# Kernel tuning notes

Measured on AMD Instinct MI355X. Metric: run time of the kernel, lower is better.

The kernel has to match this reference:

```python
import jax, jax.numpy as jnp
import numpy as np

TEMP = 0.2
EPS = 1e-12  # F.normalize eps


def setup_inputs() -> dict:
    key = jax.random.key(0)
    k1, k2 = jax.random.split(key)
    l, B, K, D = 4, 64, 32, 128
    emb_i = jax.random.normal(k1, (l, B, K, D), dtype=jnp.float32)
    emb_j = jax.random.normal(k2, (l, B, K, D), dtype=jnp.float32)
    joint_valid = jnp.ones((B, K), dtype=jnp.float32)
    return {"emb_i": emb_i, "emb_j": emb_j, "joint_valid": joint_valid}


def _l2norm(x):
    n = jnp.sqrt(jnp.sum(x * x, axis=-1, keepdims=True))
    return x / jnp.maximum(n, EPS)


def reference(emb_i, emb_j, joint_valid):
    l, B, K, D = emb_i.shape
    N = B * K
    z_i = _l2norm(emb_i.reshape(l, N, D))
    z_j = _l2norm(emb_j.reshape(l, N, D))
    reps = jnp.concatenate([z_i, z_j], axis=1)              # (l, 2N, D), unit rows
    # cosine similarity of unit vectors == matmul
    sim = jnp.einsum('lnd,lmd->lnm', reps, reps)            # (l, 2N, 2N)
    idx = jnp.arange(N)
    pos = sim[:, idx, idx + N]                              # diag offset +N, (l, N)
    # note: original code uses the SAME +N offset diagonal for both ij and ji
    positives = jnp.concatenate([pos, pos], axis=1)         # (l, 2N)
    neg_mask = 1.0 - jnp.eye(2 * N, dtype=sim.dtype)        # (2N, 2N)
    denom = jnp.sum(neg_mask[None] * jnp.exp(sim / TEMP), axis=2)  # (l, 2N)
    loss_partial = -jnp.log(jnp.exp(positives / TEMP) / denom)    # (l, 2N)
    joints_mask = joint_valid.reshape(1, 1, B, K)
    all_num = jnp.sum(joint_valid)
    loss = jnp.sum(loss_partial.reshape(l, 2, B, K) * joints_mask) / (2.0 * all_num)
    return loss
```

## Files before the change

kernel.cpp:

```cpp
#include <hip/hip_runtime.h>
#include <hip/hip_bf16.h>

typedef __attribute__((ext_vector_type(8))) short short8;
typedef __attribute__((ext_vector_type(4))) float floatx4;

#define NROWS 4096
#define NHALF 2048
#define DDIM  128
#define SQRT_SCALE 2.6857914f
#define LN2 0.69314718056f

#define WS_ROWPART_OFF 64
#define WS_DIAG_OFF   131136
#define WS_POS_OFF    147520
#define WS_Z_BYTE_OFF 655616

__device__ inline unsigned short f2bf(float f) {
    unsigned u = __builtin_bit_cast(unsigned, f);
    u += 0x7fffu + ((u >> 16) & 1u);
    return (unsigned short)(u >> 16);
}

__global__ __launch_bounds__(256) void k_norm(const float* __restrict__ emb_i,
                                              const float* __restrict__ emb_j,
                                              const float* __restrict__ jv,
                                              float* __restrict__ wsf,
                                              unsigned short* __restrict__ z) {
    int bx = blockIdx.x, tid = threadIdx.x;
    if (bx == 2048) {
        __shared__ float sred[256];
        float s = 0.f;
        #pragma unroll
        for (int i = 0; i < 8; ++i) s += jv[tid + 256 * i];
        sred[tid] = s; __syncthreads();
        for (int off = 128; off > 0; off >>= 1) {
            if (tid < off) sred[tid] += sred[tid + off];
            __syncthreads();
        }
        if (tid == 0) wsf[1] = sred[0];
        return;
    }
    if (bx == 0 && tid == 0) wsf[0] = 0.f;

    int wave = tid >> 6, lane = tid & 63, half = lane >> 5, sl = lane & 31;
    int r = bx * 8 + wave * 2 + half;
    int l = r >> 12, n = r & 4095;
    const float* src = (n < NHALF) ? (emb_i + ((size_t)l * NHALF + n) * DDIM)
                                   : (emb_j + ((size_t)l * NHALF + (n - NHALF)) * DDIM);
    float4 v = *(const float4*)(src + sl * 4);
    float ss = v.x * v.x + v.y * v.y + v.z * v.z + v.w * v.w;
    #pragma unroll
    for (int off = 1; off < 32; off <<= 1) ss += __shfl_xor(ss, off);
    float inv = SQRT_SCALE / fmaxf(sqrtf(ss), 1e-12f);
    unsigned p0 = ((unsigned)f2bf(v.y * inv) << 16) | (unsigned)f2bf(v.x * inv);
    unsigned p1 = ((unsigned)f2bf(v.w * inv) << 16) | (unsigned)f2bf(v.z * inv);
    *(uint2*)(z + (size_t)r * DDIM + sl * 4) = (uint2){p0, p1};
}

__global__ __launch_bounds__(256) void k_sim(const unsigned short* __restrict__ z,
                                             float* __restrict__ rowpart,
                                             float* __restrict__ diag,
                                             float* __restrict__ pos) {
    int bx = blockIdx.x, tid = threadIdx.x;
    int l = bx & 3, rb = (bx >> 2) & 15, cg = bx >> 6;
    int wave = tid >> 6, lane = tid & 63, m = lane & 15, quad = lane >> 4;
    const unsigned short* zl = z + (size_t)l * NROWS * DDIM;
    int l4 = l * NROWS;
    int R0 = rb * 256 + wave * 64;
    int C0 = cg * 512;

    short8 a[4][4];
    #pragma unroll
    for (int rs = 0; rs < 4; ++rs) {
        const unsigned short* p = zl + (size_t)(R0 + rs * 16 + m) * DDIM + quad * 8;
        #pragma unroll
        for (int kk = 0; kk < 4; ++kk) a[rs][kk] = *(const short8*)(p + kk * 32);
    }
    floatx4 rsum[4];
    #pragma unroll
    for (int rs = 0; rs < 4; ++rs) rsum[rs] = (floatx4){0.f, 0.f, 0.f, 0.f};

    const unsigned short* bp = zl + (size_t)(C0 + m) * DDIM + quad * 8;
    short8 bc[4], bn[4];
    #pragma unroll
    for (int k = 0; k < 4; ++k) bc[k] = *(const short8*)(bp + k * 32);

    #pragma unroll 2
    for (int cs = 0; cs < 32; ++cs) {
        if (cs < 31) {
            const unsigned short* q = bp + (size_t)(cs + 1) * 16 * DDIM;
            #pragma unroll
            for (int k = 0; k < 4; ++k) bn[k] = *(const short8*)(q + k * 32);
        }
        int c0 = C0 + cs * 16;
        #pragma unroll
        for (int rs = 0; rs < 4; ++rs) {
            floatx4 acc = (floatx4){0.f, 0.f, 0.f, 0.f};
            acc = __builtin_amdgcn_mfma_f32_16x16x32_bf16(a[rs][0], bc[0], acc, 0, 0, 0);
            acc = __builtin_amdgcn_mfma_f32_16x16x32_bf16(a[rs][1], bc[1], acc, 0, 0, 0);
            acc = __builtin_amdgcn_mfma_f32_16x16x32_bf16(a[rs][2], bc[2], acc, 0, 0, 0);
            acc = __builtin_amdgcn_mfma_f32_16x16x32_bf16(a[rs][3], bc[3], acc, 0, 0, 0);
            int rbase = R0 + rs * 16;
            if (c0 == rbase || c0 == (rbase ^ 2048)) {
                int c = m - (quad << 2);
                if (c >= 0 && c < 4)
                    ((c0 == rbase) ? diag : pos)[l4 + rbase + m] = acc[c];
            }
            rsum[rs][0] += __builtin_amdgcn_exp2f(acc[0]);
            rsum[rs][1] += __builtin_amdgcn_exp2f(acc[1]);
            rsum[rs][2] += __builtin_amdgcn_exp2f(acc[2]);
            rsum[rs][3] += __builtin_amdgcn_exp2f(acc[3]);
        }
        if (cs < 31) {
            #pragma unroll
            for (int k = 0; k < 4; ++k) bc[k] = bn[k];
        }
    }
    #pragma unroll
    for (int off = 1; off < 16; off <<= 1)
        #pragma unroll
        for (int rs = 0; rs < 4; ++rs)
            #pragma unroll
            for (int c = 0; c < 4; ++c)
                rsum[rs][c] += __shfl_xor(rsum[rs][c], off);
    if (m == 0) {
        #pragma unroll
        for (int rs = 0; rs < 4; ++rs)
            #pragma unroll
            for (int c = 0; c < 4; ++c) {
                int rg = R0 + rs * 16 + quad * 4 + c;
                rowpart[cg * 16384 + l4 + rg] = rsum[rs][c];
            }
    }
}

__global__ __launch_bounds__(256) void k_loss(const float* __restrict__ jv,
                                              const float* __restrict__ rowpart,
                                              const float* __restrict__ diag,
                                              const float* __restrict__ pos,
                                              float* __restrict__ wsf) {
    __shared__ float sred[256];
    int tid = threadIdx.x;
    int r = blockIdx.x * 256 + tid;
    int n = r & 4095;
    float tot = 0.f;
    #pragma unroll
    for (int g = 0; g < 8; ++g) tot += rowpart[g * 16384 + r];
    float denom = tot - __builtin_amdgcn_exp2f(diag[r]);
    float contrib = LN2 * (__builtin_amdgcn_logf(denom) - pos[r]);
    float local = contrib * jv[n & (NHALF - 1)];
    sred[tid] = local; __syncthreads();
    for (int off = 128; off > 0; off >>= 1) {
        if (tid < off) sred[tid] += sred[tid + off];
        __syncthreads();
    }
    if (tid == 0) atomicAdd(&wsf[0], sred[0]);
}

__global__ void k_final(const float* __restrict__ wsf, float* __restrict__ out) {
    if (threadIdx.x == 0) out[0] = wsf[0] / (2.f * wsf[1]);
}

extern "C" void kernel_launch(void* const* d_in, const int* in_sizes, int n_in,
                              void* d_out, int out_size, void* d_ws, size_t ws_size,
                              hipStream_t stream) {
    const float* emb_i = (const float*)d_in[0];
    const float* emb_j = (const float*)d_in[1];
    const float* jv    = (const float*)d_in[2];
    float* wsf     = (float*)d_ws;
    float* rowpart = wsf + WS_ROWPART_OFF;
    float* diag    = wsf + WS_DIAG_OFF;
    float* pos     = wsf + WS_POS_OFF;
    unsigned short* z = (unsigned short*)((char*)d_ws + WS_Z_BYTE_OFF);
    float* out = (float*)d_out;

    k_norm <<<2049, 256, 0, stream>>>(emb_i, emb_j, jv, wsf, z);
    k_sim  <<<512,  256, 0, stream>>>(z, rowpart, diag, pos);
    k_loss <<<64,   256, 0, stream>>>(jv, rowpart, diag, pos, wsf);
    k_final<<<1,    64,  0, stream>>>(wsf, out);
}
```

Before: 102.6 us.

## Fuse similarity, loss and final kernels using atomic grid counters

Merges the similarity, per-row loss reduction and final division into one kernel. The first 64 blocks spin on an agent-scope atomic counter until all 512 blocks have written their row partials, then compute the loss, and the last finishing block writes the output. This removes two kernel launches and their gaps. The B-tile loop is also restructured into explicit double buffering with two register sets. The spin-wait relies on all 512 blocks being co-resident or the waiting blocks being scheduled after the others, which risks deadlock or stalls if they are not.

```diff
diff --git a/kernel.cpp b/kernel.cpp
--- a/kernel.cpp
+++ b/kernel.cpp
@@ -40,7 +40,9 @@
         if (tid == 0) wsf[1] = sred[0];
         return;
     }
-    if (bx == 0 && tid == 0) wsf[0] = 0.f;
+    if (bx == 0 && tid == 0) {
+        wsf[0] = 0.f; wsf[2] = 0.f; wsf[3] = 0.f;
+    }
 
     int wave = tid >> 6, lane = tid & 63, half = lane >> 5, sl = lane & 31;
     int r = bx * 8 + wave * 2 + half;
@@ -57,10 +59,16 @@
     *(uint2*)(z + (size_t)r * DDIM + sl * 4) = (uint2){p0, p1};
 }
 
-__global__ __launch_bounds__(256) void k_sim(const unsigned short* __restrict__ z,
-                                             float* __restrict__ rowpart,
-                                             float* __restrict__ diag,
-                                             float* __restrict__ pos) {
+__global__ __launch_bounds__(256) void k_simloss(const unsigned short* __restrict__ z,
+                                                 float* __restrict__ wsf,
+                                                 const float* __restrict__ jv,
+                                                 float* __restrict__ out) {
+    float* rowpart = wsf + WS_ROWPART_OFF;
+    float* diag    = wsf + WS_DIAG_OFF;
+    float* pos     = wsf + WS_POS_OFF;
+    unsigned* cnt  = (unsigned*)&wsf[2];
+    unsigned* cnt2 = (unsigned*)&wsf[3];
+
     int bx = blockIdx.x, tid = threadIdx.x;
     int l = bx & 3, rb = (bx >> 2) & 15, cg = bx >> 6;
     int wave = tid >> 6, lane = tid & 63, m = lane & 15, quad = lane >> 4;
@@ -80,26 +88,15 @@
     #pragma unroll
     for (int rs = 0; rs < 4; ++rs) rsum[rs] = (floatx4){0.f, 0.f, 0.f, 0.f};
 
-    const unsigned short* bp = zl + (size_t)(C0 + m) * DDIM + quad * 8;
-    short8 bc[4], bn[4];
-    #pragma unroll
-    for (int k = 0; k < 4; ++k) bc[k] = *(const short8*)(bp + k * 32);
-
-    #pragma unroll 2
-    for (int cs = 0; cs < 32; ++cs) {
-        if (cs < 31) {
-            const unsigned short* q = bp + (size_t)(cs + 1) * 16 * DDIM;
-            #pragma unroll
-            for (int k = 0; k < 4; ++k) bn[k] = *(const short8*)(q + k * 32);
-        }
-        int c0 = C0 + cs * 16;
+    auto simstep = [&](short8* B, int cs_) {
+        int c0 = C0 + cs_ * 16;
         #pragma unroll
         for (int rs = 0; rs < 4; ++rs) {
             floatx4 acc = (floatx4){0.f, 0.f, 0.f, 0.f};
-            acc = __builtin_amdgcn_mfma_f32_16x16x32_bf16(a[rs][0], bc[0], acc, 0, 0, 0);
-            acc = __builtin_amdgcn_mfma_f32_16x16x32_bf16(a[rs][1], bc[1], acc, 0, 0, 0);
-            acc = __builtin_amdgcn_mfma_f32_16x16x32_bf16(a[rs][2], bc[2], acc, 0, 0, 0);
-            acc = __builtin_amdgcn_mfma_f32_16x16x32_bf16(a[rs][3], bc[3], acc, 0, 0, 0);
+            acc = __builtin_amdgcn_mfma_f32_16x16x32_bf16(a[rs][0], B[0], acc, 0, 0, 0);
+            acc = __builtin_amdgcn_mfma_f32_16x16x32_bf16(a[rs][1], B[1], acc, 0, 0, 0);
+            acc = __builtin_amdgcn_mfma_f32_16x16x32_bf16(a[rs][2], B[2], acc, 0, 0, 0);
+            acc = __builtin_amdgcn_mfma_f32_16x16x32_bf16(a[rs][3], B[3], acc, 0, 0, 0);
             int rbase = R0 + rs * 16;
             if (c0 == rbase || c0 == (rbase ^ 2048)) {
                 int c = m - (quad << 2);
@@ -111,11 +108,26 @@
             rsum[rs][2] += __builtin_amdgcn_exp2f(acc[2]);
             rsum[rs][3] += __builtin_amdgcn_exp2f(acc[3]);
         }
-        if (cs < 31) {
+    };
+
+    const unsigned short* bp = zl + (size_t)(C0 + m) * DDIM + quad * 8;
+    short8 bA[4], bB[4];
+    #pragma unroll
+    for (int k = 0; k < 4; ++k) bA[k] = *(const short8*)(bp + k * 32);
+
+    for (int cs = 0; cs < 32; cs += 2) {
+        const unsigned short* q1 = bp + (size_t)(cs + 1) * (16 * DDIM);
+        #pragma unroll
+        for (int k = 0; k < 4; ++k) bB[k] = *(const short8*)(q1 + k * 32);
+        simstep(bA, cs);
+        if (cs + 2 < 32) {
+            const unsigned short* q2 = bp + (size_t)(cs + 2) * (16 * DDIM);
             #pragma unroll
-            for (int k = 0; k < 4; ++k) bc[k] = bn[k];
-        }
-    }
+            for (int k = 0; k < 4; ++k) bA[k] = *(const short8*)(q2 + k * 32);
+        }
+        simstep(bB, cs + 1);
+    }
+
     #pragma unroll
     for (int off = 1; off < 16; off <<= 1)
         #pragma unroll
@@ -132,16 +144,23 @@
                 rowpart[cg * 16384 + l4 + rg] = rsum[rs][c];
             }
     }
-}
-
-__global__ __launch_bounds__(256) void k_loss(const float* __restrict__ jv,
-                                              const float* __restrict__ rowpart,
-                                              const float* __restrict__ diag,
-                                              const float* __restrict__ pos,
-                                              float* __restrict__ wsf) {
+
+    __syncthreads();
+    if (tid == 0) {
+        __threadfence();
+        __hip_atomic_fetch_add(cnt, 1u, __ATOMIC_RELEASE, __HIP_MEMORY_SCOPE_AGENT);
+    }
+    if (bx >= 64) return;
+
+    if (tid == 0) {
+        while (__hip_atomic_load(cnt, __ATOMIC_ACQUIRE, __HIP_MEMORY_SCOPE_AGENT) < 512u)
+            __builtin_amdgcn_s_sleep(8);
+    }
+    __syncthreads();
+    __threadfence();
+
     __shared__ float sred[256];
-    int tid = threadIdx.x;
-    int r = blockIdx.x * 256 + tid;
+    int r = bx * 256 + tid;
     int n = r & 4095;
     float tot = 0.f;
     #pragma unroll
@@ -154,11 +173,16 @@
         if (tid < off) sred[tid] += sred[tid + off];
         __syncthreads();
     }
-    if (tid == 0) atomicAdd(&wsf[0], sred[0]);
-}
-
-__global__ void k_final(const float* __restrict__ wsf, float* __restrict__ out) {
-    if (threadIdx.x == 0) out[0] = wsf[0] / (2.f * wsf[1]);
+    if (tid == 0) {
+        atomicAdd(&wsf[0], sred[0]);
+        __threadfence();
+        unsigned old = __hip_atomic_fetch_add(cnt2, 1u, __ATOMIC_ACQ_REL,
+                                              __HIP_MEMORY_SCOPE_AGENT);
+        if (old == 63u) {
+            float s = atomicAdd(&wsf[0], 0.f);
+            out[0] = s / (2.f * wsf[1]);
+        }
+    }
 }
 
 extern "C" void kernel_launch(void* const* d_in, const int* in_sizes, int n_in,
@@ -167,15 +191,10 @@
     const float* emb_i = (const float*)d_in[0];
     const float* emb_j = (const float*)d_in[1];
     const float* jv    = (const float*)d_in[2];
-    float* wsf     = (float*)d_ws;
-    float* rowpart = wsf + WS_ROWPART_OFF;
-    float* diag    = wsf + WS_DIAG_OFF;
-    float* pos     = wsf + WS_POS_OFF;
+    float* wsf = (float*)d_ws;
     unsigned short* z = (unsigned short*)((char*)d_ws + WS_Z_BYTE_OFF);
     float* out = (float*)d_out;
 
-    k_norm <<<2049, 256, 0, stream>>>(emb_i, emb_j, jv, wsf, z);
-    k_sim  <<<512,  256, 0, stream>>>(z, rowpart, diag, pos);
-    k_loss <<<64,   256, 0, stream>>>(jv, rowpart, diag, pos, wsf);
-    k_final<<<1,    64,  0, stream>>>(wsf, out);
-}
+    k_norm   <<<2049, 256, 0, stream>>>(emb_i, emb_j, jv, wsf, z);
+    k_simloss<<<512,  256, 0, stream>>>(z, wsf, jv, out);
+}
```

After: 123.6 us. 1.2x slower.
